# Kernel tuning notes

Hardware: AMD Instinct MI355X
Metric: run time of the kernel (lower is better)

The kernel has to match this reference:

```python
import math
import jax, jax.numpy as jnp
import numpy as np

H_HEADS = 8
K_MAX = 64
MIN_WINDOW = 1.0
SHARPNESS = 5.0


def rmsnorm(x, w, eps=1e-6):
    x32 = x.astype(jnp.float32)
    var = jnp.mean(x32 * x32, axis=-1, keepdims=True)
    return (w * (x32 * jax.lax.rsqrt(var + eps))).astype(x.dtype)


def setup_inputs() -> dict:
    key = jax.random.key(0)
    ks = jax.random.split(key, 12)
    B, L, C = 1, 4096, 256
    H, K = H_HEADS, K_MAX
    s = 0.02
    return {
        "x": jax.random.normal(ks[0], (B, L, C), jnp.float32),
        "window_w": jax.random.normal(ks[1], (C, H), jnp.float32) * s,
        "window_b": jnp.zeros((H,), jnp.float32),
        "window_gamma": jnp.ones((H,), jnp.float32),
        "offset_w": jax.random.normal(ks[2], (C, H), jnp.float32) * s,
        "offset_b": jnp.zeros((H,), jnp.float32),
        "offset_gamma": jnp.ones((H,), jnp.float32),
        "kernel_w": jax.random.normal(ks[3], (C, H * K), jnp.float32) * s,
        "kernel_b": jnp.zeros((H * K,), jnp.float32),
        "kernel_gamma": jnp.ones((H * K,), jnp.float32),
        "v_w": jax.random.normal(ks[4], (C, C), jnp.float32) * (1.0 / math.sqrt(C)),
        "v_b": jnp.zeros((C,), jnp.float32),
        "out_w": jax.random.normal(ks[5], (C, C), jnp.float32) * s,
    }


def reference(x, window_w, window_b, window_gamma, offset_w, offset_b, offset_gamma,
              kernel_w, kernel_b, kernel_gamma, v_w, v_b, out_w):
    B, L, C = x.shape
    H, K = H_HEADS, K_MAX
    D = C // H
    max_window = min(int(math.sqrt(L)), K)
    half = max_window // 2
    max_offset = int(math.sqrt(L))
    N = 2 * half + 1  # num_offsets

    # per-position learned window sizes, center offsets, kernel weights
    window_raw = jax.nn.sigmoid(rmsnorm(x @ window_w + window_b, window_gamma))
    window_sizes = MIN_WINDOW + window_raw * (max_window - MIN_WINDOW)      # [B,L,H]
    center_offsets = jnp.tanh(rmsnorm(x @ offset_w + offset_b, offset_gamma)) * max_offset  # [B,L,H]
    kernel_weights = jax.nn.silu(rmsnorm(x @ kernel_w + kernel_b, kernel_gamma)).reshape(B, L, H, K)
    v = (x @ v_w + v_b).reshape(B, L, H, D)

    local = jnp.arange(-half, half + 1, dtype=x.dtype)                      # [N]
    positions = jnp.arange(L, dtype=x.dtype).reshape(1, L, 1, 1)
    neighbor = positions + center_offsets[..., None] + local.reshape(1, 1, 1, N)  # [B,L,H,N]
    valid = (neighbor >= 0) & (neighbor < L)
    nclamp = jnp.clip(neighbor, 0, L - 1)

    rel = jnp.abs(local).reshape(1, 1, 1, N) / (window_sizes[..., None] / 2 + 1e-6)
    window_mask = jax.nn.sigmoid(SHARPNESS * (1.0 - rel)) * valid.astype(x.dtype)

    # kernel interpolation by relative distance
    kidx = jnp.clip(rel, 0, 1) * (K - 1)
    i_fl = jnp.clip(kidx.astype(jnp.int32), 0, K - 2)                       # [B,L,H,N]
    i_ce = i_fl + 1
    w_ce = kidx - i_fl.astype(x.dtype)
    k_fl = jnp.take_along_axis(kernel_weights, i_fl, axis=-1)
    k_ce = jnp.take_along_axis(kernel_weights, i_ce, axis=-1)
    kernel_interp = k_fl * (1.0 - w_ce) + k_ce * w_ce

    attn = kernel_interp * window_mask
    attn = attn / (jnp.sum(attn, axis=-1, keepdims=True) + 1e-6)            # [B,L,H,N]

    # bilinear gather of values at fractional neighbor positions
    p_fl = jnp.clip(jnp.floor(nclamp).astype(jnp.int32), 0, L - 1)
    p_ce = jnp.clip(p_fl + 1, 0, L - 1)
    frac = nclamp - p_fl.astype(x.dtype)                                    # [B,L,H,N]

    v_bh = v.transpose(0, 2, 1, 3)                                          # [B,H,L,D]
    idx_f = p_fl.transpose(0, 2, 1, 3).reshape(B, H, L * N)
    idx_c = p_ce.transpose(0, 2, 1, 3).reshape(B, H, L * N)
    v_fl = jnp.take_along_axis(v_bh, idx_f[..., None], axis=2).reshape(B, H, L, N, D)
    v_ce = jnp.take_along_axis(v_bh, idx_c[..., None], axis=2).reshape(B, H, L, N, D)
    frac_bh = frac.transpose(0, 2, 1, 3)[..., None]                         # [B,H,L,N,1]
    v_nb = v_fl * (1.0 - frac_bh) + v_ce * frac_bh                          # [B,H,L,N,D]

    attn_bh = attn.transpose(0, 2, 1, 3)                                    # [B,H,L,N]
    out = jnp.einsum('bhln,bhlnd->bhld', attn_bh, v_nb)                     # [B,H,L,D]
    out = out.transpose(0, 2, 1, 3).reshape(B, L, C)
    return jax.nn.silu(out @ out_w)
```

## Files before the change

### kernel.cpp

```cpp
#include <hip/hip_runtime.h>
#include <math.h>

#define L_SEQ 4096
#define C_DIM 256
#define H_HEADS 8
#define K_MAX 64
#define D_HEAD 32
#define HALF_W 32
#define N_OFF 65
#define HK 512

__device__ __forceinline__ float sigmoidf_(float x) { return 1.0f / (1.0f + expf(-x)); }

__global__ void __launch_bounds__(256, 2)
proj_gemm(const float* __restrict__ A, const float* __restrict__ kw_w,
          const float* __restrict__ vw, const float* __restrict__ kb,
          const float* __restrict__ vb,
          float* __restrict__ kwbuf, float* __restrict__ vbuf) {
    __shared__ float As[16][132];
    __shared__ float Bs[16][68];

    const int tid = threadIdx.x;
    const int tx = tid & 15;
    const int ty = tid >> 4;
    const int l0 = blockIdx.y * 128;
    const int n0 = blockIdx.x * 64;

    const int ar0 = tid >> 2;
    const int ac0 = (tid & 3) * 4;
    const int ar1 = ar0 + 64;
    const int bk = tid >> 4;
    const int bn = (tid & 15) * 4;

    const float* Bsrc;
    int ldb, coff;
    if (n0 < 512) { Bsrc = kw_w; ldb = 512; coff = n0; }
    else          { Bsrc = vw;   ldb = 256; coff = n0 - 512; }

    float acc[8][4];
#pragma unroll
    for (int i = 0; i < 8; ++i)
#pragma unroll
        for (int jj = 0; jj < 4; ++jj) acc[i][jj] = 0.0f;

    float4 av0 = *(const float4*)&A[(l0 + ar0) * C_DIM + ac0];
    float4 av1 = *(const float4*)&A[(l0 + ar1) * C_DIM + ac0];
    float4 bv  = *(const float4*)&Bsrc[bk * ldb + coff + bn];

    for (int k0 = 0; k0 < C_DIM; k0 += 16) {
        __syncthreads();
        As[ac0 + 0][ar0] = av0.x;
        As[ac0 + 1][ar0] = av0.y;
        As[ac0 + 2][ar0] = av0.z;
        As[ac0 + 3][ar0] = av0.w;
        As[ac0 + 0][ar1] = av1.x;
        As[ac0 + 1][ar1] = av1.y;
        As[ac0 + 2][ar1] = av1.z;
        As[ac0 + 3][ar1] = av1.w;
        *(float4*)&Bs[bk][bn] = bv;
        __syncthreads();
        if (k0 + 16 < C_DIM) {
            av0 = *(const float4*)&A[(l0 + ar0) * C_DIM + (k0 + 16) + ac0];
            av1 = *(const float4*)&A[(l0 + ar1) * C_DIM + (k0 + 16) + ac0];
            bv  = *(const float4*)&Bsrc[(k0 + 16 + bk) * ldb + coff + bn];
        }
#pragma unroll
        for (int kk = 0; kk < 16; ++kk) {
            const float4 a4lo = *(const float4*)&As[kk][ty * 8];
            const float4 a4hi = *(const float4*)&As[kk][ty * 8 + 4];
            const float4 b4   = *(const float4*)&Bs[kk][tx * 4];
            const float ar[8] = {a4lo.x, a4lo.y, a4lo.z, a4lo.w,
                                 a4hi.x, a4hi.y, a4hi.z, a4hi.w};
            const float br[4] = {b4.x, b4.y, b4.z, b4.w};
#pragma unroll
            for (int i = 0; i < 8; ++i)
#pragma unroll
                for (int jj = 0; jj < 4; ++jj)
                    acc[i][jj] = fmaf(ar[i], br[jj], acc[i][jj]);
        }
    }

    const int g0 = n0 + tx * 4;
    float4 bz;
    float* dst;
    int stride, col;
    if (g0 < 512) { bz = *(const float4*)&kb[g0];       dst = kwbuf; stride = 512; col = g0; }
    else          { bz = *(const float4*)&vb[g0 - 512]; dst = vbuf;  stride = 256; col = g0 - 512; }
#pragma unroll
    for (int i = 0; i < 8; ++i) {
        const int row = l0 + ty * 8 + i;
        float4 o;
        o.x = acc[i][0] + bz.x;
        o.y = acc[i][1] + bz.y;
        o.z = acc[i][2] + bz.z;
        o.w = acc[i][3] + bz.w;
        *(float4*)&dst[row * stride + col] = o;
    }
}

__global__ void __launch_bounds__(256, 2)
conv_fused(const float* __restrict__ x,
           const float* __restrict__ ww, const float* __restrict__ wb,
           const float* __restrict__ wg,
           const float* __restrict__ ow, const float* __restrict__ ob,
           const float* __restrict__ og,
           const float* __restrict__ kg,
           const float* __restrict__ kwraw, const float* __restrict__ v,
           float* __restrict__ out) {
    const int l = blockIdx.x;
    const int tid = threadIdx.x;

    __shared__ float red[256];
    __shared__ float rs_s;
    __shared__ float kwrow[HK];
    __shared__ float wsz[H_HEADS], ofs[H_HEADS];
    __shared__ float4 tap[H_HEADS][N_OFF];
    __shared__ float2 warr[H_HEADS][N_OFF + 1];
    __shared__ float inv_denom[H_HEADS];
    __shared__ int okflag;

    if (tid == 0) okflag = 1;

    {
        const int j = tid;
        const float* row = kwraw + l * HK;
        const float z0 = row[j];
        const float z1 = row[j + 256];
        red[j] = z0 * z0 + z1 * z1;
        __syncthreads();
        for (int s = 128; s > 0; s >>= 1) {
            if (j < s) red[j] += red[j + s];
            __syncthreads();
        }
        if (j == 0) rs_s = rsqrtf(red[0] / (float)HK + 1e-6f);
        __syncthreads();
        const float rs = rs_s;
        const float n0v = kg[j] * z0 * rs;
        const float n1v = kg[j + 256] * z1 * rs;
        kwrow[j]       = n0v * sigmoidf_(n0v);
        kwrow[j + 256] = n1v * sigmoidf_(n1v);
    }

    if (tid < 64) {
        const int lane = tid;
        const float* xr = x + l * C_DIM;
        float accw[H_HEADS], acco[H_HEADS];
#pragma unroll
        for (int h = 0; h < H_HEADS; ++h) { accw[h] = 0.0f; acco[h] = 0.0f; }
#pragma unroll
        for (int i = 0; i < C_DIM / 64; ++i) {
            const int c = lane + i * 64;
            const float xv = xr[c];
            const float* wwc = ww + c * H_HEADS;
            const float* owc = ow + c * H_HEADS;
#pragma unroll
            for (int h = 0; h < H_HEADS; ++h) {
                accw[h] = fmaf(xv, wwc[h], accw[h]);
                acco[h] = fmaf(xv, owc[h], acco[h]);
            }
        }
#pragma unroll
        for (int off = 32; off > 0; off >>= 1) {
#pragma unroll
            for (int h = 0; h < H_HEADS; ++h) {
                accw[h] += __shfl_xor(accw[h], off);
                acco[h] += __shfl_xor(acco[h], off);
            }
        }
        if (lane < H_HEADS) {
            float zw[H_HEADS], zo[H_HEADS];
            float ssw = 0.0f, sso = 0.0f;
#pragma unroll
            for (int h = 0; h < H_HEADS; ++h) {
                zw[h] = accw[h] + wb[h];
                zo[h] = acco[h] + ob[h];
                ssw += zw[h] * zw[h];
                sso += zo[h] * zo[h];
            }
            const float rw = rsqrtf(ssw / (float)H_HEADS + 1e-6f);
            const float ro = rsqrtf(sso / (float)H_HEADS + 1e-6f);
            const float nw = wg[lane] * zw[lane] * rw;
            const float no = og[lane] * zo[lane] * ro;
            wsz[lane] = 1.0f + sigmoidf_(nw) * 63.0f;
            ofs[lane] = tanhf(no) * 64.0f;
        }
    }
    __syncthreads();

    for (int t = tid; t < H_HEADS * N_OFF; t += 256) {
        const int h = t / N_OFF;
        const int n = t - h * N_OFF;
        const float ws  = wsz[h];
        const float off = ofs[h];
        const float local = (float)(n - HALF_W);
        const float neighbor = (float)l + off + local;
        const bool valid = (neighbor >= 0.0f) && (neighbor < (float)L_SEQ);
        const float nc = fminf(fmaxf(neighbor, 0.0f), (float)(L_SEQ - 1));

        const float rel = fabsf(local) / (ws * 0.5f + 1e-6f);
        const float mask = sigmoidf_(5.0f * (1.0f - rel)) * (valid ? 1.0f : 0.0f);

        const float kidx = fminf(rel, 1.0f) * (float)(K_MAX - 1);
        int ifl = (int)kidx;
        ifl = min(ifl, K_MAX - 2);
        const float wce = kidx - (float)ifl;
        const float kf = kwrow[h * K_MAX + ifl];
        const float kc = kwrow[h * K_MAX + ifl + 1];
        const float attnv = (kf * (1.0f - wce) + kc * wce) * mask;

        int p = (int)floorf(nc);
        p = min(max(p, 0), L_SEQ - 1);
        const int pc = min(p + 1, L_SEQ - 1);
        const float fr = nc - (float)p;

        float4 tv;
        tv.x = attnv;
        tv.y = fr;
        tv.z = __int_as_float(p * C_DIM + h * D_HEAD);
        tv.w = __int_as_float(pc * C_DIM + h * D_HEAD);
        tap[h][n] = tv;
    }
    __syncthreads();

    for (int t = tid; t < H_HEADS * (N_OFF + 1); t += 256) {
        const int h = t / (N_OFF + 1);
        const int m = t - h * (N_OFF + 1);
        float w, rowf;
        if (m == 0) {
            const float4 cur = tap[h][0];
            w = cur.x * (1.0f - cur.y);
            rowf = cur.z;
        } else {
            const float4 prev = tap[h][m - 1];
            const float wc = prev.x * prev.y;
            if (m < N_OFF) {
                const float4 cur = tap[h][m];
                w = cur.x * (1.0f - cur.y) + wc;
                rowf = cur.z;
                if (wc != 0.0f && __float_as_int(prev.w) != __float_as_int(cur.z))
                    okflag = 0;
            } else {
                w = wc;
                rowf = prev.w;
            }
        }
        warr[h][m] = make_float2(w, rowf);
    }

    if (tid < H_HEADS) {
        float s = 0.0f;
        for (int n = 0; n < N_OFF; ++n) s += tap[tid][n].x;
        inv_denom[tid] = 1.0f / (s + 1e-6f);
    }
    __syncthreads();

    const int h = tid >> 5;
    const int d = tid & 31;
    float acc = 0.0f;
    if (okflag) {
#pragma unroll 6
        for (int m = 0; m < N_OFF + 1; ++m) {
            const float2 t2 = warr[h][m];
            acc = fmaf(t2.x, v[__float_as_int(t2.y) + d], acc);
        }
    } else {
#pragma unroll 5
        for (int n = 0; n < N_OFF; ++n) {
            const float4 t4 = tap[h][n];
            const int bf = __float_as_int(t4.z);
            const int bc = __float_as_int(t4.w);
            const float vf = v[bf + d];
            const float vc = v[bc + d];
            acc = fmaf(t4.x, fmaf(t4.y, vc - vf, vf), acc);
        }
    }
    out[l * C_DIM + h * D_HEAD + d] = acc * inv_denom[h];
}

__global__ void __launch_bounds__(256, 4)
out_gemm(const float* __restrict__ A, const float* __restrict__ W,
         float* __restrict__ out) {
    __shared__ float As[16][68];
    __shared__ float Bs[16][68];

    const int tid = threadIdx.x;
    const int tx = tid & 15;
    const int ty = tid >> 4;
    const int l0 = blockIdx.y * 64;
    const int n0 = blockIdx.x * 64;

    const int am = tid >> 2;
    const int ak = (tid & 3) * 4;
    const int bk = tid >> 4;
    const int bn = (tid & 15) * 4;

    float acc[4][4];
#pragma unroll
    for (int i = 0; i < 4; ++i)
#pragma unroll
        for (int jj = 0; jj < 4; ++jj) acc[i][jj] = 0.0f;

    float4 av = *(const float4*)&A[(l0 + am) * C_DIM + ak];
    float4 bv = *(const float4*)&W[bk * C_DIM + n0 + bn];

    for (int k0 = 0; k0 < C_DIM; k0 += 16) {
        __syncthreads();
        As[ak + 0][am] = av.x;
        As[ak + 1][am] = av.y;
        As[ak + 2][am] = av.z;
        As[ak + 3][am] = av.w;
        *(float4*)&Bs[bk][bn] = bv;
        __syncthreads();
        if (k0 + 16 < C_DIM) {
            av = *(const float4*)&A[(l0 + am) * C_DIM + (k0 + 16) + ak];
            bv = *(const float4*)&W[(k0 + 16 + bk) * C_DIM + n0 + bn];
        }
#pragma unroll
        for (int kk = 0; kk < 16; ++kk) {
            const float4 a4 = *(const float4*)&As[kk][ty * 4];
            const float4 b4 = *(const float4*)&Bs[kk][tx * 4];
            const float ar[4] = {a4.x, a4.y, a4.z, a4.w};
            const float br[4] = {b4.x, b4.y, b4.z, b4.w};
#pragma unroll
            for (int i = 0; i < 4; ++i)
#pragma unroll
                for (int jj = 0; jj < 4; ++jj)
                    acc[i][jj] = fmaf(ar[i], br[jj], acc[i][jj]);
        }
    }

    const int g0 = n0 + tx * 4;
#pragma unroll
    for (int i = 0; i < 4; ++i) {
        const int row = l0 + ty * 4 + i;
        float4 o;
        o.x = acc[i][0] * sigmoidf_(acc[i][0]);
        o.y = acc[i][1] * sigmoidf_(acc[i][1]);
        o.z = acc[i][2] * sigmoidf_(acc[i][2]);
        o.w = acc[i][3] * sigmoidf_(acc[i][3]);
        *(float4*)&out[row * C_DIM + g0] = o;
    }
}

extern "C" void kernel_launch(void* const* d_in, const int* in_sizes, int n_in,
                              void* d_out, int out_size, void* d_ws, size_t ws_size,
                              hipStream_t stream) {
    const float* x    = (const float*)d_in[0];
    const float* ww   = (const float*)d_in[1];
    const float* wb   = (const float*)d_in[2];
    const float* wg   = (const float*)d_in[3];
    const float* ow   = (const float*)d_in[4];
    const float* ob   = (const float*)d_in[5];
    const float* og   = (const float*)d_in[6];
    const float* kw_w = (const float*)d_in[7];
    const float* kb   = (const float*)d_in[8];
    const float* kg   = (const float*)d_in[9];
    const float* vw   = (const float*)d_in[10];
    const float* vb   = (const float*)d_in[11];
    const float* outw = (const float*)d_in[12];
    float* y = (float*)d_out;

    float* ws_f    = (float*)d_ws;
    float* kwbuf   = ws_f;
    float* vbuf    = kwbuf + L_SEQ * HK;
    float* convbuf = vbuf + L_SEQ * C_DIM;

    proj_gemm<<<dim3(12, L_SEQ / 128), 256, 0, stream>>>(x, kw_w, vw, kb, vb, kwbuf, vbuf);
    conv_fused<<<L_SEQ, 256, 0, stream>>>(x, ww, wb, wg, ow, ob, og, kg, kwbuf, vbuf, convbuf);
    out_gemm<<<dim3(C_DIM / 64, L_SEQ / 64), 256, 0, stream>>>(convbuf, outw, y);
}
```

Before: 149.4 us.

## Process two sequence positions per conv block with split-role warps

The conv_fused kernel now handles two positions per block, halving the grid. Threads 0-127 compute the window/offset projections for both rows while threads 128-255 load the kernel-weight rows, and the RMS reduction is replaced by a shared-memory plus shuffle reduction with fewer barriers. The gather loop interleaves two independent accumulators to expose more memory-level parallelism. In exchange the block uses more shared memory and registers, which may reduce occupancy, and the okflag is now shared across both rows.

Result: slower. 158.9 us (+6.3%).

```diff
diff --git a/kernel.cpp b/kernel.cpp
--- a/kernel.cpp
+++ b/kernel.cpp
@@ -107,43 +107,36 @@
            const float* __restrict__ kg,
            const float* __restrict__ kwraw, const float* __restrict__ v,
            float* __restrict__ out) {
-    const int l = blockIdx.x;
+    const int l0 = blockIdx.x * 2;
     const int tid = threadIdx.x;
 
-    __shared__ float red[256];
-    __shared__ float rs_s;
-    __shared__ float kwrow[HK];
-    __shared__ float wsz[H_HEADS], ofs[H_HEADS];
-    __shared__ float4 tap[H_HEADS][N_OFF];
-    __shared__ float2 warr[H_HEADS][N_OFF + 1];
-    __shared__ float inv_denom[H_HEADS];
+    __shared__ float2 red2[256];
+    __shared__ float2 rs_s2;
+    __shared__ float kwrow[2][HK];
+    __shared__ float wsz[2][H_HEADS], ofs[2][H_HEADS];
+    __shared__ float4 tap[2][H_HEADS][N_OFF];
+    __shared__ float2 warr[2][H_HEADS][N_OFF + 1];
+    __shared__ float inv_denom[2][H_HEADS];
     __shared__ int okflag;
 
     if (tid == 0) okflag = 1;
 
-    {
-        const int j = tid;
-        const float* row = kwraw + l * HK;
-        const float z0 = row[j];
-        const float z1 = row[j + 256];
-        red[j] = z0 * z0 + z1 * z1;
-        __syncthreads();
-        for (int s = 128; s > 0; s >>= 1) {
-            if (j < s) red[j] += red[j + s];
-            __syncthreads();
-        }
-        if (j == 0) rs_s = rsqrtf(red[0] / (float)HK + 1e-6f);
-        __syncthreads();
-        const float rs = rs_s;
-        const float n0v = kg[j] * z0 * rs;
-        const float n1v = kg[j + 256] * z1 * rs;
-        kwrow[j]       = n0v * sigmoidf_(n0v);
-        kwrow[j + 256] = n1v * sigmoidf_(n1v);
-    }
-
-    if (tid < 64) {
-        const int lane = tid;
-        const float* xr = x + l * C_DIM;
+    float z00a = 0, z00b = 0, z01a = 0, z01b = 0;
+    float z10a = 0, z10b = 0, z11a = 0, z11b = 0;
+    if (tid >= 128) {
+        const int j0 = tid - 128, j1 = tid;
+        const float* r0 = kwraw + l0 * HK;
+        const float* r1 = kwraw + (l0 + 1) * HK;
+        z00a = r0[j0]; z00b = r0[j0 + 256];
+        z01a = r0[j1]; z01b = r0[j1 + 256];
+        z10a = r1[j0]; z10b = r1[j0 + 256];
+        z11a = r1[j1]; z11b = r1[j1 + 256];
+        red2[j0] = make_float2(z00a * z00a + z00b * z00b, z10a * z10a + z10b * z10b);
+        red2[j1] = make_float2(z01a * z01a + z01b * z01b, z11a * z11a + z11b * z11b);
+    } else {
+        const int r = tid >> 6;
+        const int lane = tid & 63;
+        const float* xr = x + (l0 + r) * C_DIM;
         float accw[H_HEADS], acco[H_HEADS];
 #pragma unroll
         for (int h = 0; h < H_HEADS; ++h) { accw[h] = 0.0f; acco[h] = 0.0f; }
@@ -181,17 +174,54 @@
             const float ro = rsqrtf(sso / (float)H_HEADS + 1e-6f);
             const float nw = wg[lane] * zw[lane] * rw;
             const float no = og[lane] * zo[lane] * ro;
-            wsz[lane] = 1.0f + sigmoidf_(nw) * 63.0f;
-            ofs[lane] = tanhf(no) * 64.0f;
-        }
-    }
-    __syncthreads();
-
-    for (int t = tid; t < H_HEADS * N_OFF; t += 256) {
-        const int h = t / N_OFF;
-        const int n = t - h * N_OFF;
-        const float ws  = wsz[h];
-        const float off = ofs[h];
+            wsz[r][lane] = 1.0f + sigmoidf_(nw) * 63.0f;
+            ofs[r][lane] = tanhf(no) * 64.0f;
+        }
+    }
+    __syncthreads();
+
+    if (tid < 128) {
+        const float2 a = red2[tid], b = red2[tid + 128];
+        red2[tid] = make_float2(a.x + b.x, a.y + b.y);
+    }
+    __syncthreads();
+    if (tid < 64) {
+        float sx = red2[tid].x + red2[tid + 64].x;
+        float sy = red2[tid].y + red2[tid + 64].y;
+#pragma unroll
+        for (int off = 32; off > 0; off >>= 1) {
+            sx += __shfl_xor(sx, off);
+            sy += __shfl_xor(sy, off);
+        }
+        if (tid == 0)
+            rs_s2 = make_float2(rsqrtf(sx / (float)HK + 1e-6f),
+                                rsqrtf(sy / (float)HK + 1e-6f));
+    }
+    __syncthreads();
+
+    if (tid >= 128) {
+        const int j0 = tid - 128, j1 = tid;
+        const float rs0 = rs_s2.x, rs1 = rs_s2.y;
+        float n;
+        n = kg[j0]       * z00a * rs0; kwrow[0][j0]       = n * sigmoidf_(n);
+        n = kg[j0 + 256] * z00b * rs0; kwrow[0][j0 + 256] = n * sigmoidf_(n);
+        n = kg[j1]       * z01a * rs0; kwrow[0][j1]       = n * sigmoidf_(n);
+        n = kg[j1 + 256] * z01b * rs0; kwrow[0][j1 + 256] = n * sigmoidf_(n);
+        n = kg[j0]       * z10a * rs1; kwrow[1][j0]       = n * sigmoidf_(n);
+        n = kg[j0 + 256] * z10b * rs1; kwrow[1][j0 + 256] = n * sigmoidf_(n);
+        n = kg[j1]       * z11a * rs1; kwrow[1][j1]       = n * sigmoidf_(n);
+        n = kg[j1 + 256] * z11b * rs1; kwrow[1][j1 + 256] = n * sigmoidf_(n);
+    }
+    __syncthreads();
+
+    for (int t = tid; t < 2 * H_HEADS * N_OFF; t += 256) {
+        const int r = t / (H_HEADS * N_OFF);
+        const int t2 = t - r * (H_HEADS * N_OFF);
+        const int h = t2 / N_OFF;
+        const int n = t2 - h * N_OFF;
+        const int l = l0 + r;
+        const float ws  = wsz[r][h];
+        const float off = ofs[r][h];
         const float local = (float)(n - HALF_W);
         const float neighbor = (float)l + off + local;
         const bool valid = (neighbor >= 0.0f) && (neighbor < (float)L_SEQ);
@@ -204,8 +234,8 @@
         int ifl = (int)kidx;
         ifl = min(ifl, K_MAX - 2);
         const float wce = kidx - (float)ifl;
-        const float kf = kwrow[h * K_MAX + ifl];
-        const float kc = kwrow[h * K_MAX + ifl + 1];
+        const float kf = kwrow[r][h * K_MAX + ifl];
+        const float kc = kwrow[r][h * K_MAX + ifl + 1];
         const float attnv = (kf * (1.0f - wce) + kc * wce) * mask;
 
         int p = (int)floorf(nc);
@@ -218,63 +248,71 @@
         tv.y = fr;
         tv.z = __int_as_float(p * C_DIM + h * D_HEAD);
         tv.w = __int_as_float(pc * C_DIM + h * D_HEAD);
-        tap[h][n] = tv;
-    }
-    __syncthreads();
-
-    for (int t = tid; t < H_HEADS * (N_OFF + 1); t += 256) {
-        const int h = t / (N_OFF + 1);
-        const int m = t - h * (N_OFF + 1);
-        float w, rowf;
-        if (m == 0) {
-            const float4 cur = tap[h][0];
-            w = cur.x * (1.0f - cur.y);
-            rowf = cur.z;
-        } else {
-            const float4 prev = tap[h][m - 1];
-            const float wc = prev.x * prev.y;
-            if (m < N_OFF) {
-                const float4 cur = tap[h][m];
-                w = cur.x * (1.0f - cur.y) + wc;
+        tap[r][h][n] = tv;
+    }
+    __syncthreads();
+
+    if (tid < 16) {
+        const int r = tid >> 3, h = tid & 7;
+        float s = 0.0f;
+        for (int n = 0; n < N_OFF; ++n) s += tap[r][h][n].x;
+        inv_denom[r][h] = 1.0f / (s + 1e-6f);
+    } else {
+        for (int t = tid - 16; t < 2 * H_HEADS * (N_OFF + 1); t += 240) {
+            const int r = t / (H_HEADS * (N_OFF + 1));
+            const int t2 = t - r * (H_HEADS * (N_OFF + 1));
+            const int h = t2 / (N_OFF + 1);
+            const int m = t2 - h * (N_OFF + 1);
+            float w, rowf;
+            if (m == 0) {
+                const float4 cur = tap[r][h][0];
+                w = cur.x * (1.0f - cur.y);
                 rowf = cur.z;
-                if (wc != 0.0f && __float_as_int(prev.w) != __float_as_int(cur.z))
-                    okflag = 0;
             } else {
-                w = wc;
-                rowf = prev.w;
+                const float4 prev = tap[r][h][m - 1];
+                const float wc = prev.x * prev.y;
+                if (m < N_OFF) {
+                    const float4 cur = tap[r][h][m];
+                    w = cur.x * (1.0f - cur.y) + wc;
+                    rowf = cur.z;
+                    if (wc != 0.0f && __float_as_int(prev.w) != __float_as_int(cur.z))
+                        okflag = 0;
+                } else {
+                    w = wc;
+                    rowf = prev.w;
+                }
             }
-        }
-        warr[h][m] = make_float2(w, rowf);
-    }
-
-    if (tid < H_HEADS) {
-        float s = 0.0f;
-        for (int n = 0; n < N_OFF; ++n) s += tap[tid][n].x;
-        inv_denom[tid] = 1.0f / (s + 1e-6f);
+            warr[r][h][m] = make_float2(w, rowf);
+        }
     }
     __syncthreads();
 
     const int h = tid >> 5;
     const int d = tid & 31;
-    float acc = 0.0f;
+    float acc0 = 0.0f, acc1 = 0.0f;
     if (okflag) {
-#pragma unroll 6
+#pragma unroll 3
         for (int m = 0; m < N_OFF + 1; ++m) {
-            const float2 t2 = warr[h][m];
-            acc = fmaf(t2.x, v[__float_as_int(t2.y) + d], acc);
+            const float2 ta = warr[0][h][m];
+            const float2 tb = warr[1][h][m];
+            acc0 = fmaf(ta.x, v[__float_as_int(ta.y) + d], acc0);
+            acc1 = fmaf(tb.x, v[__float_as_int(tb.y) + d], acc1);
         }
     } else {
-#pragma unroll 5
+#pragma unroll 3
         for (int n = 0; n < N_OFF; ++n) {
-            const float4 t4 = tap[h][n];
-            const int bf = __float_as_int(t4.z);
-            const int bc = __float_as_int(t4.w);
-            const float vf = v[bf + d];
-            const float vc = v[bc + d];
-            acc = fmaf(t4.x, fmaf(t4.y, vc - vf, vf), acc);
-        }
-    }
-    out[l * C_DIM + h * D_HEAD + d] = acc * inv_denom[h];
+            const float4 t4a = tap[0][h][n];
+            const float4 t4b = tap[1][h][n];
+            float vf = v[__float_as_int(t4a.z) + d];
+            float vc = v[__float_as_int(t4a.w) + d];
+            acc0 = fmaf(t4a.x, fmaf(t4a.y, vc - vf, vf), acc0);
+            vf = v[__float_as_int(t4b.z) + d];
+            vc = v[__float_as_int(t4b.w) + d];
+            acc1 = fmaf(t4b.x, fmaf(t4b.y, vc - vf, vf), acc1);
+        }
+    }
+    out[l0 * C_DIM + h * D_HEAD + d]       = acc0 * inv_denom[0][h];
+    out[(l0 + 1) * C_DIM + h * D_HEAD + d] = acc1 * inv_denom[1][h];
 }
 
 __global__ void __launch_bounds__(256, 4)
@@ -366,6 +404,6 @@
     float* convbuf = vbuf + L_SEQ * C_DIM;
 
     proj_gemm<<<dim3(12, L_SEQ / 128), 256, 0, stream>>>(x, kw_w, vw, kb, vb, kwbuf, vbuf);
-    conv_fused<<<L_SEQ, 256, 0, stream>>>(x, ww, wb, wg, ow, ob, og, kg, kwbuf, vbuf, convbuf);
+    conv_fused<<<L_SEQ / 2, 256, 0, stream>>>(x, ww, wb, wg, ow, ob, og, kg, kwbuf, vbuf, convbuf);
     out_gemm<<<dim3(C_DIM / 64, L_SEQ / 64), 256, 0, stream>>>(convbuf, outw, y);
 }
```
